# Optimization experiments

Measured on AMD Instinct MI355X. Metric: run time of the kernel, lower is better.

The kernel has to match this reference:

```python
import jax, jax.numpy as jnp
import numpy as np
import math

H = 8  # num_heads
SCALE = 1.0 / math.sqrt(512.0)  # original divides by sqrt(dim_V), not sqrt(head_dim)


def setup_inputs() -> dict:
    key = jax.random.key(0)
    ks = jax.random.split(key, 16)
    B, N, D = 32, 512, 512
    s = 1.0 / math.sqrt(D)
    return {
        "Q": jax.random.normal(ks[0], (B, N, D), jnp.float32),
        "K": jax.random.normal(ks[1], (B, N, D), jnp.float32),
        "Wq": jax.random.normal(ks[2], (D, D), jnp.float32) * s,
        "bq": jnp.zeros((D,), jnp.float32),
        "Wk": jax.random.normal(ks[3], (D, D), jnp.float32) * s,
        "bk": jnp.zeros((D,), jnp.float32),
        "Wv": jax.random.normal(ks[4], (D, D), jnp.float32) * s,
        "bv": jnp.zeros((D,), jnp.float32),
        "Wo": jax.random.normal(ks[5], (D, D), jnp.float32) * s,
        "bo": jnp.zeros((D,), jnp.float32),
        "W1": jax.random.normal(ks[6], (D, D), jnp.float32) * s,
        "b1": jnp.zeros((D,), jnp.float32),
        "W2": jax.random.normal(ks[7], (D, D), jnp.float32) * s,
        "b2": jnp.zeros((D,), jnp.float32),
    }


def reference(Q, K, Wq, bq, Wk, bk, Wv, bv, Wo, bo, W1, b1, W2, b2):
    B, Nq, D = Q.shape
    dh = D // H
    # projections (torch Linear: x @ W.T + b)
    q = (Q @ Wq.T + bq).reshape(B, Nq, H, dh)
    k = (K @ Wk.T + bk).reshape(B, K.shape[1], H, dh)
    v = (K @ Wv.T + bv).reshape(B, K.shape[1], H, dh)
    # scores: [B, H, Nq, Nk], scaled by 1/sqrt(dim_V)
    scores = jnp.einsum("bqhd,bkhd->bhqk", q, k) * SCALE
    # NOTE: original softmax is over dim=1 of [H*B, Nq, Nk] == the QUERY axis
    A = jax.nn.softmax(scores, axis=2)
    attn = jnp.einsum("bhqk,bkhd->bqhd", A, v).reshape(B, Nq, D)
    out = Q + (attn @ Wo.T + bo)  # dropout p=0.0
    ffn = jax.nn.relu(out @ W1.T + b1) @ W2.T + b2
    return out + ffn
```

## Files before the change

### kernel.cpp

```cpp
#include <hip/hip_runtime.h>
#include <stdint.h>

#define SCALE_ 0.044194173824159216f

typedef __attribute__((ext_vector_type(8))) short bf16x8;
typedef __attribute__((ext_vector_type(4))) float f32x4;

__device__ __forceinline__ ushort f2b(float f) {
  union { float f; uint32_t u; } v; v.f = f;
  return (ushort)((v.u + 0x7fffu + ((v.u >> 16) & 1u)) >> 16);
}
__device__ __forceinline__ uint32_t cvtpk(float lo, float hi) {
  uint32_t r; asm("v_cvt_pk_bf16_f32 %0, %1, %2" : "=v"(r) : "v"(lo), "v"(hi)); return r;
}
__device__ __forceinline__ void gld16(void* lds, const void* g) {
  __builtin_amdgcn_global_load_lds(
      (const __attribute__((address_space(1))) uint32_t*)g,
      (__attribute__((address_space(3))) uint32_t*)lds, 16, 0, 0);
}

__global__ __launch_bounds__(256)
void k_cvt(const float* __restrict__ Q, const float* __restrict__ K,
           const float* __restrict__ w0, const float* __restrict__ w1,
           const float* __restrict__ w2, const float* __restrict__ w3,
           const float* __restrict__ w4, const float* __restrict__ w5,
           ushort* __restrict__ Qb, ushort* __restrict__ Kb, ushort* __restrict__ Wb)
{
  const long long NQ = 8388608LL, NW = 262144LL;
  long long i = ((long long)blockIdx.x * 256 + threadIdx.x) * 4;
  const float* src; ushort* dst; long long off;
  if (i < NQ)        { src = Q; dst = Qb; off = i; }
  else if (i < 2*NQ) { src = K; dst = Kb; off = i - NQ; }
  else {
    long long j = i - 2*NQ; int seg = (int)(j / NW); off = j - (long long)seg * NW;
    switch (seg) { case 0: src = w0; break; case 1: src = w1; break; case 2: src = w2; break;
                   case 3: src = w3; break; case 4: src = w4; break; default: src = w5; }
    dst = Wb + (size_t)seg * NW;
  }
  float4 v = *(const float4*)(src + off);
  ushort4 o = make_ushort4(f2b(v.x), f2b(v.y), f2b(v.z), f2b(v.w));
  *(ushort4*)(dst + off) = o;
}

template<int EPI>
__device__ __forceinline__ void gemm_body(const ushort* __restrict__ A, const ushort* __restrict__ Bw,
                                          const float* __restrict__ bias, const float* __restrict__ extra,
                                          float* __restrict__ outf, ushort* __restrict__ outb,
                                          char* lds, int m0, int n0)
{
  const int t = threadIdx.x;
  const int w = t >> 6, lane = t & 63;
  const int wm = w >> 1, wn = w & 1;
  const int rA = lane & 15, g = lane >> 4;

  const ushort* srcA[4]; int ldsA[4];
#pragma unroll
  for (int j = 0; j < 4; j++) {
    int L = (t + j*512) * 16;
    int U = L ^ (((L >> 7) & 7) << 4);
    srcA[j] = A + (size_t)(m0 + (U >> 7))*512 + ((U & 127) >> 1);
    ldsA[j] = L;
  }
  const ushort* srcB[2]; int ldsB[2];
#pragma unroll
  for (int j = 0; j < 2; j++) {
    int L = (t + j*512) * 16;
    int U = L ^ (((L >> 7) & 7) << 4);
    srcB[j] = Bw + (size_t)(n0 + (U >> 7))*512 + ((U & 127) >> 1);
    ldsB[j] = 32768 + L;
  }

#define STAGE_A(ti) do { char* bb_ = lds + ((ti) % 3) * 49152; \
    _Pragma("unroll") \
    for (int j = 0; j < 4; j++) gld16(bb_ + ldsA[j], srcA[j] + (ti)*64); } while (0)
#define STAGE_B(ti) do { char* bb_ = lds + ((ti) % 3) * 49152; \
    _Pragma("unroll") \
    for (int j = 0; j < 2; j++) gld16(bb_ + ldsB[j], srcB[j] + (ti)*64); } while (0)

  STAGE_A(0); STAGE_B(0);
  STAGE_A(1); STAGE_B(1);

  f32x4 acc[4][4] = {};
  for (int i = 0; i < 8; i++) {
    if (i < 7) asm volatile("s_waitcnt vmcnt(6)" ::: "memory");
    else       asm volatile("s_waitcnt vmcnt(0)" ::: "memory");
    __builtin_amdgcn_s_barrier();
    __builtin_amdgcn_sched_barrier(0);
    const char* bufc = lds + (i % 3) * 49152;

    bf16x8 afA[4], bfA[4];
#pragma unroll
    for (int m = 0; m < 4; m++) {
      int row = wm*64 + m*16 + rA;
      afA[m] = *(const bf16x8*)(bufc + ((row*128 + g*16) ^ ((row & 7) << 4)));
    }
#pragma unroll
    for (int n = 0; n < 4; n++) {
      int row = wn*64 + n*16 + rA;
      bfA[n] = *(const bf16x8*)(bufc + 32768 + ((row*128 + g*16) ^ ((row & 7) << 4)));
    }
    if (i < 6) STAGE_A(i + 2);
    __builtin_amdgcn_s_barrier();
    __builtin_amdgcn_sched_barrier(0);

    bf16x8 afB[4], bfB[4];
#pragma unroll
    for (int m = 0; m < 4; m++) {
      int row = wm*64 + m*16 + rA;
      afB[m] = *(const bf16x8*)(bufc + ((row*128 + 64 + g*16) ^ ((row & 7) << 4)));
    }
#pragma unroll
    for (int n = 0; n < 4; n++) {
      int row = wn*64 + n*16 + rA;
      bfB[n] = *(const bf16x8*)(bufc + 32768 + ((row*128 + 64 + g*16) ^ ((row & 7) << 4)));
    }
    if (i < 6) STAGE_B(i + 2);
    __builtin_amdgcn_s_setprio(1);
#pragma unroll
    for (int m = 0; m < 4; m++)
#pragma unroll
      for (int n = 0; n < 4; n++)
        acc[m][n] = __builtin_amdgcn_mfma_f32_16x16x32_bf16(afA[m], bfA[n], acc[m][n], 0, 0, 0);
    __builtin_amdgcn_s_setprio(0);
    __builtin_amdgcn_s_barrier();
    __builtin_amdgcn_sched_barrier(0);

    __builtin_amdgcn_s_setprio(1);
#pragma unroll
    for (int m = 0; m < 4; m++)
#pragma unroll
      for (int n = 0; n < 4; n++)
        acc[m][n] = __builtin_amdgcn_mfma_f32_16x16x32_bf16(afB[m], bfB[n], acc[m][n], 0, 0, 0);
    __builtin_amdgcn_s_setprio(0);
  }
#undef STAGE_A
#undef STAGE_B

#pragma unroll
  for (int m = 0; m < 4; m++)
#pragma unroll
    for (int n = 0; n < 4; n++) {
      int col = n0 + wn*64 + n*16 + rA;
      float bb = bias[col];
      if (EPI == 4) {
        int b = m0 >> 9, k0 = m0 & 511;
        int hh = col >> 6, dl = col & 63;
        int kg = k0 + wm*64 + m*16 + g*4;
        float v0 = acc[m][n][0] + bb, v1 = acc[m][n][1] + bb;
        float v2 = acc[m][n][2] + bb, v3 = acc[m][n][3] + bb;
        uint2 pk;
        pk.x = (uint32_t)f2b(v0) | ((uint32_t)f2b(v1) << 16);
        pk.y = (uint32_t)f2b(v2) | ((uint32_t)f2b(v3) << 16);
        *(uint2*)(outb + ((size_t)((b*8 + hh)*64 + dl)*512 + kg)) = pk;
      } else {
#pragma unroll
        for (int r = 0; r < 4; r++) {
          int row = m0 + wm*64 + m*16 + g*4 + r;
          size_t idx = (size_t)row*512 + col;
          float v = acc[m][n][r] + bb;
          if (EPI == 0)      outb[idx] = f2b(v);
          else if (EPI == 1) { float o = extra[idx] + v; outf[idx] = o; outb[idx] = f2b(o); }
          else if (EPI == 2) outb[idx] = f2b(v > 0.f ? v : 0.f);
          else               outf[idx] += v;
        }
      }
    }
}

template<int EPI>
__global__ __launch_bounds__(512, 2)
void k_gemm(const ushort* __restrict__ A, const ushort* __restrict__ Bw,
            const float* __restrict__ bias, const float* __restrict__ extra,
            float* __restrict__ outf, ushort* __restrict__ outb)
{
  __shared__ __align__(16) char lds[3*49152];
  gemm_body<EPI>(A, Bw, bias, extra, outf, outb, lds, blockIdx.x*256, blockIdx.y*128);
}

__global__ __launch_bounds__(512, 2)
void k_gemm_qkv(const ushort* __restrict__ Qb, const ushort* __restrict__ Kb,
                const ushort* __restrict__ Wb, const float* __restrict__ bq,
                const float* __restrict__ bk, const float* __restrict__ bvv,
                ushort* __restrict__ qkout, ushort* __restrict__ vpT)
{
  __shared__ __align__(16) char lds[3*49152];
  int z = blockIdx.z;
  if (z == 2) {
    gemm_body<4>(Kb, Wb + 2*(size_t)262144, bvv, nullptr, nullptr,
                 vpT, lds, blockIdx.x*256, blockIdx.y*128);
  } else {
    const ushort* A = (z == 0) ? Qb : Kb;
    const float* bias = (z == 0) ? bq : bk;
    gemm_body<0>(A, Wb + (size_t)z*262144, bias, nullptr, nullptr,
                 qkout + (size_t)z*8388608, lds, blockIdx.x*256, blockIdx.y*128);
  }
}

__global__ __launch_bounds__(256, 2)
void k_z(const ushort* __restrict__ qp, const ushort* __restrict__ kp, float* __restrict__ zinv)
{
  __shared__ __align__(16) ushort qt[2*8192];
  int bid = blockIdx.x;
  int bh = bid >> 1, kh = bid & 1;
  int b = bh >> 3, h = bh & 7;
  int t = threadIdx.x, w = t >> 6, lane = t & 63;
  int rA = lane & 15, g = lane >> 4;
  const ushort* qbase = qp + (size_t)(b*512)*512 + h*64;
  bf16x8 kf[4][2];
#pragma unroll
  for (int n = 0; n < 4; n++)
#pragma unroll
    for (int ks = 0; ks < 2; ks++)
      kf[n][ks] = *(const bf16x8*)(kp + (size_t)(b*512 + kh*256 + w*64 + n*16 + rA)*512 + h*64 + ks*32 + g*8);

#define Z_STAGE(buf, qb) do { \
    _Pragma("unroll") \
    for (int i = 0; i < 4; i++) { \
      int c = i*256 + w*64 + lane; \
      int row = c >> 3, sl = c & 7; \
      gld16((char*)qt + (buf)*16384 + i*4096 + w*1024, \
            qbase + (size_t)((qb)*128 + row)*512 + ((sl ^ (row & 7))*8)); } } while (0)

  Z_STAGE(0, 0);
  __syncthreads();
  float Zacc[4] = {0.f, 0.f, 0.f, 0.f};
  for (int qb = 0; qb < 4; qb++) {
    const int cur = qb & 1;
    if (qb < 3) Z_STAGE(cur ^ 1, qb + 1);
    const ushort* qtb = qt + cur*8192;
    f32x4 acc[8][4] = {};
#pragma unroll
    for (int ks = 0; ks < 2; ks++) {
      bf16x8 af[8];
#pragma unroll
      for (int m = 0; m < 8; m++) {
        int q = m*16 + rA;
        af[m] = *(const bf16x8*)(qtb + q*64 + (((ks*4 + g) ^ (q & 7))*8));
      }
      __builtin_amdgcn_s_setprio(1);
#pragma unroll
      for (int m = 0; m < 8; m++)
#pragma unroll
        for (int n = 0; n < 4; n++)
          acc[m][n] = __builtin_amdgcn_mfma_f32_16x16x32_bf16(af[m], kf[n][ks], acc[m][n], 0, 0, 0);
      __builtin_amdgcn_s_setprio(0);
    }
#pragma unroll
    for (int m = 0; m < 8; m++)
#pragma unroll
      for (int n = 0; n < 4; n++) {
        float s = 0.f;
#pragma unroll
        for (int r = 0; r < 4; r++) s += __expf(acc[m][n][r] * SCALE_);
        Zacc[n] += s;
      }
    __syncthreads();
  }
#undef Z_STAGE
#pragma unroll
  for (int n = 0; n < 4; n++) {
    float v = Zacc[n];
    v += __shfl_xor(v, 16);
    v += __shfl_xor(v, 32);
    if (lane < 16) zinv[(size_t)bh*512 + kh*256 + w*64 + n*16 + lane] = 1.0f / v;
  }
}

__global__ __launch_bounds__(256, 2)
void k_attn(const ushort* __restrict__ qp, const ushort* __restrict__ kp,
            const ushort* __restrict__ vpT, const float* __restrict__ zinv,
            ushort* __restrict__ attn)
{
  __shared__ __align__(16) ushort kt2[2*4096];
  __shared__ __align__(16) ushort vt2[2*4096];
  __shared__ __align__(16) ushort P[4*4096];
  __shared__ float zl[512];
  int bid = blockIdx.x;
  int bh = bid >> 1, qh = bid & 1;
  int b = bh >> 3, h = bh & 7;
  int t = threadIdx.x, w = t >> 6, lane = t & 63;
  int rA = lane & 15, g = lane >> 4;
  const ushort* kbase = kp + (size_t)(b*512)*512 + h*64;
  const ushort* vbase = vpT + (size_t)bh*64*512;
  ushort* Pw = P + w*4096;
  bf16x8 qf[4][2];
#pragma unroll
  for (int m = 0; m < 4; m++)
#pragma unroll
    for (int ks = 0; ks < 2; ks++)
      qf[m][ks] = *(const bf16x8*)(qp + (size_t)(b*512 + qh*256 + w*64 + m*16 + rA)*512 + h*64 + ks*32 + g*8);

#define A_STAGE(buf, kc) do { \
    _Pragma("unroll") \
    for (int i = 0; i < 2; i++) { \
      int c = i*256 + w*64 + lane; \
      { int k = c >> 3, sl = c & 7; \
        gld16((char*)kt2 + (buf)*8192 + i*4096 + w*1024, \
              kbase + (size_t)((kc)*64 + k)*512 + ((sl ^ (k & 7))*8)); } \
      { int d = c >> 3, sl = c & 7; \
        gld16((char*)vt2 + (buf)*8192 + i*4096 + w*1024, \
              vbase + (size_t)d*512 + (kc)*64 + ((sl ^ (d & 7))*8)); } } } while (0)

  A_STAGE(0, 0);
  zl[t]       = zinv[(size_t)bh*512 + t];
  zl[t + 256] = zinv[(size_t)bh*512 + t + 256];
  __syncthreads();
  f32x4 oacc[4][4] = {};
  for (int kc = 0; kc < 8; kc++) {
    const int cur = kc & 1;
    if (kc < 7) A_STAGE(cur ^ 1, kc + 1);
    const ushort* ktb = kt2 + cur*4096;
    const ushort* vtb = vt2 + cur*4096;
#pragma unroll
    for (int knh = 0; knh < 2; knh++) {
      f32x4 sacc[2][4] = {};
#pragma unroll
      for (int ks = 0; ks < 2; ks++) {
        bf16x8 kfr[2];
#pragma unroll
        for (int kn2 = 0; kn2 < 2; kn2++) {
          int k = (knh*2 + kn2)*16 + rA;
          kfr[kn2] = *(const bf16x8*)(ktb + k*64 + (((ks*4 + g) ^ (k & 7))*8));
        }
        __builtin_amdgcn_s_setprio(1);
#pragma unroll
        for (int kn2 = 0; kn2 < 2; kn2++)
#pragma unroll
          for (int m = 0; m < 4; m++)
            sacc[kn2][m] = __builtin_amdgcn_mfma_f32_16x16x32_bf16(kfr[kn2], qf[m][ks], sacc[kn2][m], 0, 0, 0);
        __builtin_amdgcn_s_setprio(0);
      }
#pragma unroll
      for (int kn2 = 0; kn2 < 2; kn2++) {
        int kn = knh*2 + kn2;
        f32x4 zv = *(const f32x4*)&zl[kc*64 + kn*16 + g*4];
#pragma unroll
        for (int m = 0; m < 4; m++) {
          float e0 = __expf(sacc[kn2][m][0] * SCALE_) * zv[0];
          float e1 = __expf(sacc[kn2][m][1] * SCALE_) * zv[1];
          float e2 = __expf(sacc[kn2][m][2] * SCALE_) * zv[2];
          float e3 = __expf(sacc[kn2][m][3] * SCALE_) * zv[3];
          uint2 pk; pk.x = cvtpk(e0, e1); pk.y = cvtpk(e2, e3);
          int q = m*16 + rA;
          int kb2 = kn*32 + g*8;
          *(uint2*)((char*)Pw + q*128 + (kb2 ^ ((q & 7) << 4))) = pk;
        }
      }
    }
#pragma unroll
    for (int ks = 0; ks < 2; ks++) {
      bf16x8 pa[4], vb[4];
#pragma unroll
      for (int m = 0; m < 4; m++) {
        int q = m*16 + rA;
        pa[m] = *(const bf16x8*)((const char*)Pw + q*128 + ((ks*64 + g*16) ^ ((q & 7) << 4)));
      }
#pragma unroll
      for (int n = 0; n < 4; n++) {
        int d = n*16 + rA;
        vb[n] = *(const bf16x8*)((const char*)vtb + d*128 + ((ks*64 + g*16) ^ ((d & 7) << 4)));
      }
      __builtin_amdgcn_s_setprio(1);
#pragma unroll
      for (int m = 0; m < 4; m++)
#pragma unroll
        for (int n = 0; n < 4; n++)
          oacc[m][n] = __builtin_amdgcn_mfma_f32_16x16x32_bf16(pa[m], vb[n], oacc[m][n], 0, 0, 0);
      __builtin_amdgcn_s_setprio(0);
    }
    __syncthreads();
  }
#undef A_STAGE
#pragma unroll
  for (int m = 0; m < 4; m++)
#pragma unroll
    for (int n = 0; n < 4; n++)
#pragma unroll
      for (int r = 0; r < 4; r++) {
        int q = qh*256 + w*64 + m*16 + g*4 + r;
        int dcol = h*64 + n*16 + rA;
        attn[(size_t)(b*512 + q)*512 + dcol] = f2b(oacc[m][n][r]);
      }
}

extern "C" void kernel_launch(void* const* d_in, const int* in_sizes, int n_in,
                              void* d_out, int out_size, void* d_ws, size_t ws_size,
                              hipStream_t stream) {
  const float* Q  = (const float*)d_in[0];
  const float* K  = (const float*)d_in[1];
  const float* Wq = (const float*)d_in[2];
  const float* bq = (const float*)d_in[3];
  const float* Wk = (const float*)d_in[4];
  const float* bk = (const float*)d_in[5];
  const float* Wv = (const float*)d_in[6];
  const float* bv = (const float*)d_in[7];
  const float* Wo = (const float*)d_in[8];
  const float* bo = (const float*)d_in[9];
  const float* W1 = (const float*)d_in[10];
  const float* b1 = (const float*)d_in[11];
  const float* W2 = (const float*)d_in[12];
  const float* b2 = (const float*)d_in[13];
  float* out = (float*)d_out;

  const size_t SZ = (size_t)16384 * 512;
  ushort* Qb   = (ushort*)d_ws;
  ushort* Kb   = Qb + SZ;
  ushort* qp   = Kb + SZ;
  ushort* kp   = qp + SZ;
  ushort* vpT  = kp + SZ;
  ushort* Wb   = vpT + SZ;
  float*  zinv = (float*)(Wb + 6 * (size_t)262144);
  ushort* attn = Qb;
  ushort* outb = Kb;
  ushort* h1   = vpT;

  k_cvt<<<dim3(17920), dim3(256), 0, stream>>>(Q, K, Wq, Wk, Wv, Wo, W1, W2, Qb, Kb, Wb);
  k_gemm_qkv<<<dim3(64, 4, 3), dim3(512), 0, stream>>>(Qb, Kb, Wb, bq, bk, bv, qp, vpT);
  k_z<<<dim3(512), dim3(256), 0, stream>>>(qp, kp, zinv);
  k_attn<<<dim3(512), dim3(256), 0, stream>>>(qp, kp, vpT, zinv, attn);
  k_gemm<1><<<dim3(64, 4), dim3(512), 0, stream>>>(attn, Wb + 3*(size_t)262144, bo, Q, out, outb);
  k_gemm<2><<<dim3(64, 4), dim3(512), 0, stream>>>(outb, Wb + 4*(size_t)262144, b1, nullptr, nullptr, h1);
  k_gemm<3><<<dim3(64, 4), dim3(512), 0, stream>>>(h1, Wb + 5*(size_t)262144, b2, nullptr, out, nullptr);
}
```

Before: 164.9 us.

## Fuse softmax normalizer and attention kernels into one per-head block with resident K/V

Merges the separate column-sum (Z) kernel and the attention kernel into a single kernel with one 512-thread block per (batch, head). The whole K and V^T tile for that head is loaded into LDS once and reused for both the normalizer pass and the P·V pass. The Q staging buffer is reused as per-wave P scratch, with manual vmcnt waits and barriers replacing __syncthreads. This removes a kernel launch and the duplicated global reads of K, Q and V. In exchange it needs about 160KB of LDS per block, allowing only one block per CU, and it round-trips zinv through global memory inside the block.

```diff
diff --git a/kernel.cpp b/kernel.cpp
--- a/kernel.cpp
+++ b/kernel.cpp
@@ -196,38 +196,59 @@
   }
 }
 
-__global__ __launch_bounds__(256, 2)
-void k_z(const ushort* __restrict__ qp, const ushort* __restrict__ kp, float* __restrict__ zinv)
+__global__ __launch_bounds__(512, 2)
+void k_att2(const ushort* __restrict__ qp, const ushort* __restrict__ kp,
+            const ushort* __restrict__ vpT, float* __restrict__ zinv,
+            ushort* __restrict__ attn)
 {
-  __shared__ __align__(16) ushort qt[2*8192];
-  int bid = blockIdx.x;
-  int bh = bid >> 1, kh = bid & 1;
+  __shared__ __align__(16) char kt[65536];
+  __shared__ __align__(16) char vt[65536];
+  __shared__ __align__(16) char qpr[32768];
+  int bh = blockIdx.x;
   int b = bh >> 3, h = bh & 7;
   int t = threadIdx.x, w = t >> 6, lane = t & 63;
   int rA = lane & 15, g = lane >> 4;
+  const ushort* kbase = kp + (size_t)(b*512)*512 + h*64;
   const ushort* qbase = qp + (size_t)(b*512)*512 + h*64;
+  const ushort* vbase = vpT + (size_t)bh*64*512;
+
+#pragma unroll
+  for (int i = 0; i < 8; i++) {
+    int c = i*512 + t; int row = c >> 3, sl = c & 7;
+    gld16(kt + c*16, kbase + (size_t)row*512 + ((sl ^ (row & 7))*8));
+  }
+#define STAGE_Q(buf, qb) do { \
+    _Pragma("unroll") \
+    for (int i = 0; i < 2; i++) { \
+      int c = i*512 + t; int row = c >> 3, sl = c & 7; \
+      gld16(qpr + (buf)*16384 + c*16, \
+            qbase + (size_t)((qb)*128 + row)*512 + ((sl ^ (row & 7))*8)); } } while (0)
+  STAGE_Q(0, 0);
+  STAGE_Q(1, 1);
+#pragma unroll
+  for (int i = 0; i < 8; i++) {
+    int c = i*512 + t; int d = c >> 6, sl = c & 63;
+    gld16(vt + c*16, vbase + (size_t)d*512 + ((sl ^ (d & 7))*8));
+  }
+
+  asm volatile("s_waitcnt vmcnt(10)" ::: "memory");
+  __builtin_amdgcn_s_barrier();
+  __builtin_amdgcn_sched_barrier(0);
   bf16x8 kf[4][2];
 #pragma unroll
   for (int n = 0; n < 4; n++)
 #pragma unroll
-    for (int ks = 0; ks < 2; ks++)
-      kf[n][ks] = *(const bf16x8*)(kp + (size_t)(b*512 + kh*256 + w*64 + n*16 + rA)*512 + h*64 + ks*32 + g*8);
-
-#define Z_STAGE(buf, qb) do { \
-    _Pragma("unroll") \
-    for (int i = 0; i < 4; i++) { \
-      int c = i*256 + w*64 + lane; \
-      int row = c >> 3, sl = c & 7; \
-      gld16((char*)qt + (buf)*16384 + i*4096 + w*1024, \
-            qbase + (size_t)((qb)*128 + row)*512 + ((sl ^ (row & 7))*8)); } } while (0)
-
-  Z_STAGE(0, 0);
-  __syncthreads();
+    for (int ks = 0; ks < 2; ks++) {
+      int k = w*64 + n*16 + rA;
+      kf[n][ks] = *(const bf16x8*)(kt + k*128 + (((ks*4 + g) ^ (k & 7))*16));
+    }
   float Zacc[4] = {0.f, 0.f, 0.f, 0.f};
   for (int qb = 0; qb < 4; qb++) {
-    const int cur = qb & 1;
-    if (qb < 3) Z_STAGE(cur ^ 1, qb + 1);
-    const ushort* qtb = qt + cur*8192;
+    if (qb == 1)      { asm volatile("s_waitcnt vmcnt(10)" ::: "memory"); }
+    else if (qb == 2) { asm volatile("s_waitcnt vmcnt(2)" ::: "memory"); }
+    else if (qb == 3) { asm volatile("s_waitcnt vmcnt(0)" ::: "memory"); }
+    if (qb) { __builtin_amdgcn_s_barrier(); __builtin_amdgcn_sched_barrier(0); }
+    const char* qtb = qpr + (qb & 1)*16384;
     f32x4 acc[8][4] = {};
 #pragma unroll
     for (int ks = 0; ks < 2; ks++) {
@@ -235,7 +256,7 @@
 #pragma unroll
       for (int m = 0; m < 8; m++) {
         int q = m*16 + rA;
-        af[m] = *(const bf16x8*)(qtb + q*64 + (((ks*4 + g) ^ (q & 7))*8));
+        af[m] = *(const bf16x8*)(qtb + q*128 + (((ks*4 + g) ^ (q & 7))*16));
       }
       __builtin_amdgcn_s_setprio(1);
 #pragma unroll
@@ -245,6 +266,8 @@
           acc[m][n] = __builtin_amdgcn_mfma_f32_16x16x32_bf16(af[m], kf[n][ks], acc[m][n], 0, 0, 0);
       __builtin_amdgcn_s_setprio(0);
     }
+    if (qb < 3) __builtin_amdgcn_s_barrier();
+    if (qb < 2) STAGE_Q(qb & 1, qb + 2);
 #pragma unroll
     for (int m = 0; m < 8; m++)
 #pragma unroll
@@ -254,130 +277,86 @@
         for (int r = 0; r < 4; r++) s += __expf(acc[m][n][r] * SCALE_);
         Zacc[n] += s;
       }
-    __syncthreads();
-  }
-#undef Z_STAGE
+  }
+#undef STAGE_Q
 #pragma unroll
   for (int n = 0; n < 4; n++) {
     float v = Zacc[n];
     v += __shfl_xor(v, 16);
     v += __shfl_xor(v, 32);
-    if (lane < 16) zinv[(size_t)bh*512 + kh*256 + w*64 + n*16 + lane] = 1.0f / v;
-  }
-}
-
-__global__ __launch_bounds__(256, 2)
-void k_attn(const ushort* __restrict__ qp, const ushort* __restrict__ kp,
-            const ushort* __restrict__ vpT, const float* __restrict__ zinv,
-            ushort* __restrict__ attn)
-{
-  __shared__ __align__(16) ushort kt2[2*4096];
-  __shared__ __align__(16) ushort vt2[2*4096];
-  __shared__ __align__(16) ushort P[4*4096];
-  __shared__ float zl[512];
-  int bid = blockIdx.x;
-  int bh = bid >> 1, qh = bid & 1;
-  int b = bh >> 3, h = bh & 7;
-  int t = threadIdx.x, w = t >> 6, lane = t & 63;
-  int rA = lane & 15, g = lane >> 4;
-  const ushort* kbase = kp + (size_t)(b*512)*512 + h*64;
-  const ushort* vbase = vpT + (size_t)bh*64*512;
-  ushort* Pw = P + w*4096;
+    if (lane < 16) zinv[(size_t)bh*512 + w*64 + n*16 + lane] = 1.0f / v;
+  }
+  asm volatile("s_waitcnt vmcnt(0)" ::: "memory");
+  __builtin_amdgcn_s_barrier();
+  __builtin_amdgcn_sched_barrier(0);
+
   bf16x8 qf[4][2];
 #pragma unroll
   for (int m = 0; m < 4; m++)
 #pragma unroll
     for (int ks = 0; ks < 2; ks++)
-      qf[m][ks] = *(const bf16x8*)(qp + (size_t)(b*512 + qh*256 + w*64 + m*16 + rA)*512 + h*64 + ks*32 + g*8);
-
-#define A_STAGE(buf, kc) do { \
-    _Pragma("unroll") \
-    for (int i = 0; i < 2; i++) { \
-      int c = i*256 + w*64 + lane; \
-      { int k = c >> 3, sl = c & 7; \
-        gld16((char*)kt2 + (buf)*8192 + i*4096 + w*1024, \
-              kbase + (size_t)((kc)*64 + k)*512 + ((sl ^ (k & 7))*8)); } \
-      { int d = c >> 3, sl = c & 7; \
-        gld16((char*)vt2 + (buf)*8192 + i*4096 + w*1024, \
-              vbase + (size_t)d*512 + (kc)*64 + ((sl ^ (d & 7))*8)); } } } while (0)
-
-  A_STAGE(0, 0);
-  zl[t]       = zinv[(size_t)bh*512 + t];
-  zl[t + 256] = zinv[(size_t)bh*512 + t + 256];
-  __syncthreads();
+      qf[m][ks] = *(const bf16x8*)(qbase + (size_t)(w*64 + m*16 + rA)*512 + ks*32 + g*8);
+  char* Pw = qpr + w*4096;
+  const float* zb = zinv + (size_t)bh*512;
   f32x4 oacc[4][4] = {};
-  for (int kc = 0; kc < 8; kc++) {
-    const int cur = kc & 1;
-    if (kc < 7) A_STAGE(cur ^ 1, kc + 1);
-    const ushort* ktb = kt2 + cur*4096;
-    const ushort* vtb = vt2 + cur*4096;
-#pragma unroll
-    for (int knh = 0; knh < 2; knh++) {
-      f32x4 sacc[2][4] = {};
-#pragma unroll
-      for (int ks = 0; ks < 2; ks++) {
-        bf16x8 kfr[2];
-#pragma unroll
-        for (int kn2 = 0; kn2 < 2; kn2++) {
-          int k = (knh*2 + kn2)*16 + rA;
-          kfr[kn2] = *(const bf16x8*)(ktb + k*64 + (((ks*4 + g) ^ (k & 7))*8));
-        }
-        __builtin_amdgcn_s_setprio(1);
-#pragma unroll
-        for (int kn2 = 0; kn2 < 2; kn2++)
-#pragma unroll
-          for (int m = 0; m < 4; m++)
-            sacc[kn2][m] = __builtin_amdgcn_mfma_f32_16x16x32_bf16(kfr[kn2], qf[m][ks], sacc[kn2][m], 0, 0, 0);
-        __builtin_amdgcn_s_setprio(0);
-      }
-#pragma unroll
-      for (int kn2 = 0; kn2 < 2; kn2++) {
-        int kn = knh*2 + kn2;
-        f32x4 zv = *(const f32x4*)&zl[kc*64 + kn*16 + g*4];
-#pragma unroll
-        for (int m = 0; m < 4; m++) {
-          float e0 = __expf(sacc[kn2][m][0] * SCALE_) * zv[0];
-          float e1 = __expf(sacc[kn2][m][1] * SCALE_) * zv[1];
-          float e2 = __expf(sacc[kn2][m][2] * SCALE_) * zv[2];
-          float e3 = __expf(sacc[kn2][m][3] * SCALE_) * zv[3];
-          uint2 pk; pk.x = cvtpk(e0, e1); pk.y = cvtpk(e2, e3);
-          int q = m*16 + rA;
-          int kb2 = kn*32 + g*8;
-          *(uint2*)((char*)Pw + q*128 + (kb2 ^ ((q & 7) << 4))) = pk;
-        }
-      }
-    }
+  for (int kc = 0; kc < 16; kc++) {
+    f32x4 sacc[2][4] = {};
 #pragma unroll
     for (int ks = 0; ks < 2; ks++) {
-      bf16x8 pa[4], vb[4];
+      bf16x8 kfr[2];
+#pragma unroll
+      for (int kn = 0; kn < 2; kn++) {
+        int k = kc*32 + kn*16 + rA;
+        kfr[kn] = *(const bf16x8*)(kt + k*128 + (((ks*4 + g) ^ (k & 7))*16));
+      }
+      __builtin_amdgcn_s_setprio(1);
+#pragma unroll
+      for (int kn = 0; kn < 2; kn++)
+#pragma unroll
+        for (int m = 0; m < 4; m++)
+          sacc[kn][m] = __builtin_amdgcn_mfma_f32_16x16x32_bf16(kfr[kn], qf[m][ks], sacc[kn][m], 0, 0, 0);
+      __builtin_amdgcn_s_setprio(0);
+    }
+#pragma unroll
+    for (int kn = 0; kn < 2; kn++) {
+      f32x4 zv = *(const f32x4*)(zb + kc*32 + kn*16 + g*4);
 #pragma unroll
       for (int m = 0; m < 4; m++) {
+        float e0 = __expf(sacc[kn][m][0] * SCALE_) * zv[0];
+        float e1 = __expf(sacc[kn][m][1] * SCALE_) * zv[1];
+        float e2 = __expf(sacc[kn][m][2] * SCALE_) * zv[2];
+        float e3 = __expf(sacc[kn][m][3] * SCALE_) * zv[3];
+        uint2 pk; pk.x = cvtpk(e0, e1); pk.y = cvtpk(e2, e3);
         int q = m*16 + rA;
-        pa[m] = *(const bf16x8*)((const char*)Pw + q*128 + ((ks*64 + g*16) ^ ((q & 7) << 4)));
-      }
-#pragma unroll
-      for (int n = 0; n < 4; n++) {
-        int d = n*16 + rA;
-        vb[n] = *(const bf16x8*)((const char*)vtb + d*128 + ((ks*64 + g*16) ^ ((d & 7) << 4)));
-      }
-      __builtin_amdgcn_s_setprio(1);
-#pragma unroll
-      for (int m = 0; m < 4; m++)
-#pragma unroll
-        for (int n = 0; n < 4; n++)
-          oacc[m][n] = __builtin_amdgcn_mfma_f32_16x16x32_bf16(pa[m], vb[n], oacc[m][n], 0, 0, 0);
-      __builtin_amdgcn_s_setprio(0);
-    }
-    __syncthreads();
-  }
-#undef A_STAGE
+        *(uint2*)(Pw + q*64 + ((kn*32 + g*8) ^ ((q & 3) << 4))) = pk;
+      }
+    }
+    bf16x8 pa[4], vb[4];
+#pragma unroll
+    for (int m = 0; m < 4; m++) {
+      int q = m*16 + rA;
+      pa[m] = *(const bf16x8*)(Pw + q*64 + ((g*16) ^ ((q & 3) << 4)));
+    }
+#pragma unroll
+    for (int n = 0; n < 4; n++) {
+      int d = n*16 + rA;
+      vb[n] = *(const bf16x8*)(vt + d*1024 + ((kc*64 + g*16) ^ ((d & 7) << 4)));
+    }
+    __builtin_amdgcn_s_setprio(1);
+#pragma unroll
+    for (int m = 0; m < 4; m++)
+#pragma unroll
+      for (int n = 0; n < 4; n++)
+        oacc[m][n] = __builtin_amdgcn_mfma_f32_16x16x32_bf16(pa[m], vb[n], oacc[m][n], 0, 0, 0);
+    __builtin_amdgcn_s_setprio(0);
+  }
 #pragma unroll
   for (int m = 0; m < 4; m++)
 #pragma unroll
     for (int n = 0; n < 4; n++)
 #pragma unroll
       for (int r = 0; r < 4; r++) {
-        int q = qh*256 + w*64 + m*16 + g*4 + r;
+        int q = w*64 + m*16 + g*4 + r;
         int dcol = h*64 + n*16 + rA;
         attn[(size_t)(b*512 + q)*512 + dcol] = f2b(oacc[m][n][r]);
       }
@@ -416,8 +395,7 @@
 
   k_cvt<<<dim3(17920), dim3(256), 0, stream>>>(Q, K, Wq, Wk, Wv, Wo, W1, W2, Qb, Kb, Wb);
   k_gemm_qkv<<<dim3(64, 4, 3), dim3(512), 0, stream>>>(Qb, Kb, Wb, bq, bk, bv, qp, vpT);
-  k_z<<<dim3(512), dim3(256), 0, stream>>>(qp, kp, zinv);
-  k_attn<<<dim3(512), dim3(256), 0, stream>>>(qp, kp, vpT, zinv, attn);
+  k_att2<<<dim3(256), dim3(512), 0, stream>>>(qp, kp, vpT, zinv, attn);
   k_gemm<1><<<dim3(64, 4), dim3(512), 0, stream>>>(attn, Wb + 3*(size_t)262144, bo, Q, out, outb);
   k_gemm<2><<<dim3(64, 4), dim3(512), 0, stream>>>(outb, Wb + 4*(size_t)262144, b1, nullptr, nullptr, h1);
   k_gemm<3><<<dim3(64, 4), dim3(512), 0, stream>>>(h1, Wb + 5*(size_t)262144, b2, nullptr, out, nullptr);
```

Result: faster. 156.6 us (-5.0%).
